# Optimization experiments

Measured on AMD Instinct MI355X. Metric: run time of the kernel, lower is better.

The kernel has to match this reference:

```python
import jax, jax.numpy as jnp
import numpy as np

B, Q, K, H = 4, 128, 1024, 256
QS, KS, DV = 256, 256, 256


def setup_inputs() -> dict:
    key = jax.random.key(0)
    k1, k2, k3, k4, k5, k6, k7 = jax.random.split(key, 7)
    return {
        "queries": jax.random.normal(k1, (B, Q, QS), dtype=jnp.float32),
        "keys": jax.random.normal(k2, (B, K, KS), dtype=jnp.float32),
        "values": jax.random.normal(k3, (B, K, DV), dtype=jnp.float32),
        "valid_lens": jax.random.randint(k4, (B,), 1, K, dtype=jnp.int64),
        "Wq": jax.random.normal(k5, (QS, H), dtype=jnp.float32) / np.sqrt(QS),
        "Wk": jax.random.normal(k6, (KS, H), dtype=jnp.float32) / np.sqrt(KS),
        "Wv": jax.random.normal(k7, (H,), dtype=jnp.float32) / np.sqrt(H),
    }


def reference(queries, keys, values, valid_lens, Wq, Wk, Wv):
    # Projections: [B,Q,H] and [B,K,H]
    q = jnp.einsum("bqe,eh->bqh", queries, Wq)
    k = jnp.einsum("bke,eh->bkh", keys, Wk)
    # Broadcast add + tanh: [B,Q,K,H] intermediate (the kernel-headroom op)
    feats = jnp.tanh(q[:, :, None, :] + k[:, None, :, :])
    # hidden -> 1 reduction: scores [B,Q,K]
    scores = jnp.einsum("bqkh,h->bqk", feats, Wv)
    # masked softmax: positions >= valid_len set to -1e6 (as in sequence_mask)
    mask = jnp.arange(scores.shape[-1])[None, None, :] < valid_lens[:, None, None]
    scores = jnp.where(mask, scores, jnp.float32(-1e6))
    attn = jax.nn.softmax(scores, axis=-1)
    # dropout is identity in eval mode
    return jnp.einsum("bqk,bkv->bqv", attn, values)
```

## Files before the change

### kernel.cpp

```cpp
#include <hip/hip_runtime.h>

#define NB 4
#define NQ 128
#define NK 1024
#define NH 256
#define NE 256
#define NV 256

#define TSCALE 2.8853900817779268f
#define LOG2E  1.4426950408889634f

static __device__ __forceinline__ float fexp2(float x){ return __builtin_amdgcn_exp2f(x); }
static __device__ __forceinline__ float frcp (float x){ return __builtin_amdgcn_rcpf(x); }
static __device__ __forceinline__ float tanh_of(float x){
    float e = fexp2(x * TSCALE);
    return fmaf(-2.0f, frcp(e + 1.0f), 1.0f);
}

__global__ __launch_bounds__(256) void proj_kernel(
    const float* __restrict__ qin, const float* __restrict__ kin,
    const float* __restrict__ Wq, const float* __restrict__ Wk,
    const float* __restrict__ Wv,
    float4* __restrict__ qdatA, float4* __restrict__ qdatB,
    float4* __restrict__ kT4) {
    const int tid = threadIdx.x;
    const int bi  = blockIdx.x;
    __shared__ float tr[NH][9];
    if (bi < NB * 32) {
        const int row0 = bi * 4;
        const float* r0 = qin + row0 * NE;
        float a0 = 0.f, a1 = 0.f, a2 = 0.f, a3 = 0.f;
#pragma unroll 2
        for (int e = 0; e < NE; e += 4) {
            float4 q0 = *(const float4*)(r0 + e);
            float4 q1 = *(const float4*)(r0 + NE + e);
            float4 q2 = *(const float4*)(r0 + 2 * NE + e);
            float4 q3 = *(const float4*)(r0 + 3 * NE + e);
#pragma unroll
            for (int j = 0; j < 4; ++j) {
                float w = Wq[(e + j) * NH + tid];
                a0 = fmaf(((const float*)&q0)[j], w, a0);
                a1 = fmaf(((const float*)&q1)[j], w, a1);
                a2 = fmaf(((const float*)&q2)[j], w, a2);
                a3 = fmaf(((const float*)&q3)[j], w, a3);
            }
        }
        float wv = Wv[tid];
        float t0 = tanh_of(a0), t1 = tanh_of(a1), t2 = tanh_of(a2), t3 = tanh_of(a3);
        qdatA[bi * NH + tid] = make_float4(t0, wv * t0, t1, wv * t1);
        qdatB[bi * NH + tid] = make_float4(t2, wv * t2, t3, wv * t3);
    } else {
        const int kb = bi - NB * 32;
        const int b  = kb >> 7;
        const int k0 = (kb & 127) * 8;
        const float* kr = kin + (b * NK + k0) * NE;
        float acc[8] = {0.f,0.f,0.f,0.f,0.f,0.f,0.f,0.f};
#pragma unroll 2
        for (int e = 0; e < NE; e += 4) {
            float4 kvv[8];
#pragma unroll
            for (int i = 0; i < 8; ++i) kvv[i] = *(const float4*)(kr + i * NE + e);
#pragma unroll
            for (int j = 0; j < 4; ++j) {
                float w = Wk[(e + j) * NH + tid];
#pragma unroll
                for (int i = 0; i < 8; ++i)
                    acc[i] = fmaf(((const float*)&kvv[i])[j], w, acc[i]);
            }
        }
#pragma unroll
        for (int i = 0; i < 8; ++i) tr[tid][i] = tanh_of(acc[i]);
        __syncthreads();
#pragma unroll
        for (int p = 0; p < 2; ++p) {
            int idx2 = p * 256 + tid;
            int hg = idx2 >> 3;
            int kk = idx2 & 7;
            float4 v = make_float4(tr[hg*4+0][kk], tr[hg*4+1][kk],
                                   tr[hg*4+2][kk], tr[hg*4+3][kk]);
            kT4[(b * 64 + hg) * NK + k0 + kk] = v;
        }
    }
}

__global__ __launch_bounds__(256) void attn_kernel(
    const float4* __restrict__ qdatA, const float4* __restrict__ qdatB,
    const float4* __restrict__ kT4, const float* __restrict__ V,
    const int* __restrict__ vlen, const float4* __restrict__ Wv4,
    float* __restrict__ part_m, float* __restrict__ part_s,
    float* __restrict__ part_pv) {
    const int tid = threadIdx.x, lane = tid & 63, wid = tid >> 6;
    const int bi = blockIdx.x;
    const int quarter = bi & 3;
    const int b  = (bi >> 2) & 3;
    const int qq = bi >> 4;
    const int vl = vlen[b];
    const int nch = (vl + 255) >> 8;
    const int pidx = (b * 32 + qq) * 4 + quarter;
    float* pm  = part_m + pidx * 4;
    float* ps  = part_s + pidx * 4;
    float* ppv = part_pv + pidx * (4 * NV);

    if (quarter >= nch) {
        if (tid < 4) { pm[tid] = -1e30f; ps[tid] = 0.0f; }
#pragma unroll
        for (int i = 0; i < 4; ++i) ppv[i * 256 + tid] = 0.0f;
        return;
    }

    __shared__ float  pw[4][NH];
    __shared__ float  pvred[4][64 * 17];
    __shared__ float  red[4][8];

    const float4* qA = qdatA + (b * 32 + qq) * NH;
    const float4* qB = qdatB + (b * 32 + qq) * NH;

    const int k = quarter * 256 + tid;
    const float4* kp = kT4 + (b * 64) * NK + k;
    float acc0 = 0.f, acc1 = 0.f, acc2 = 0.f, acc3 = 0.f;
#pragma unroll 4
    for (int h4 = 0; h4 < 64; ++h4) {
        float4 kv4 = kp[h4 * NK];
        float4 wv4 = Wv4[h4];
#pragma unroll
        for (int j = 0; j < 4; ++j) {
            float kv  = ((const float*)&kv4)[j];
            float wvb = ((const float*)&wv4)[j] * kv;
            float4 qa = qA[h4 * 4 + j];
            float4 qb = qB[h4 * 4 + j];
            acc0 = fmaf(qa.y + wvb, frcp(fmaf(qa.x, kv, 1.0f)), acc0);
            acc1 = fmaf(qa.w + wvb, frcp(fmaf(qa.z, kv, 1.0f)), acc1);
            acc2 = fmaf(qb.y + wvb, frcp(fmaf(qb.x, kv, 1.0f)), acc2);
            acc3 = fmaf(qb.w + wvb, frcp(fmaf(qb.z, kv, 1.0f)), acc3);
        }
    }
    const bool okk = k < vl;
    float s0 = okk ? acc0 : -1e30f;
    float s1 = okk ? acc1 : -1e30f;
    float s2 = okk ? acc2 : -1e30f;
    float s3 = okk ? acc3 : -1e30f;
    float m0 = s0, m1 = s1, m2 = s2, m3 = s3;
#pragma unroll
    for (int d = 32; d >= 1; d >>= 1) {
        m0 = fmaxf(m0, __shfl_xor(m0, d, 64));
        m1 = fmaxf(m1, __shfl_xor(m1, d, 64));
        m2 = fmaxf(m2, __shfl_xor(m2, d, 64));
        m3 = fmaxf(m3, __shfl_xor(m3, d, 64));
    }
    if (lane == 0) { red[wid][0]=m0; red[wid][1]=m1; red[wid][2]=m2; red[wid][3]=m3; }
    __syncthreads();
    m0 = fmaxf(fmaxf(red[0][0], red[1][0]), fmaxf(red[2][0], red[3][0]));
    m1 = fmaxf(fmaxf(red[0][1], red[1][1]), fmaxf(red[2][1], red[3][1]));
    m2 = fmaxf(fmaxf(red[0][2], red[1][2]), fmaxf(red[2][2], red[3][2]));
    m3 = fmaxf(fmaxf(red[0][3], red[1][3]), fmaxf(red[2][3], red[3][3]));
    float p0 = fexp2((s0 - m0) * LOG2E);
    float p1 = fexp2((s1 - m1) * LOG2E);
    float p2 = fexp2((s2 - m2) * LOG2E);
    float p3 = fexp2((s3 - m3) * LOG2E);
    pw[0][tid] = p0; pw[1][tid] = p1; pw[2][tid] = p2; pw[3][tid] = p3;
    float u0 = p0, u1 = p1, u2 = p2, u3 = p3;
#pragma unroll
    for (int d = 32; d >= 1; d >>= 1) {
        u0 += __shfl_xor(u0, d, 64); u1 += __shfl_xor(u1, d, 64);
        u2 += __shfl_xor(u2, d, 64); u3 += __shfl_xor(u3, d, 64);
    }
    if (lane == 0) { red[wid][4]=u0; red[wid][5]=u1; red[wid][6]=u2; red[wid][7]=u3; }
    __syncthreads();
    if (tid == 0) {
        pm[0] = m0; pm[1] = m1; pm[2] = m2; pm[3] = m3;
        ps[0] = red[0][4]+red[1][4]+red[2][4]+red[3][4];
        ps[1] = red[0][5]+red[1][5]+red[2][5]+red[3][5];
        ps[2] = red[0][6]+red[1][6]+red[2][6]+red[3][6];
        ps[3] = red[0][7]+red[1][7]+red[2][7]+red[3][7];
    }
    const float* Vb = V + (b * NK + quarter * 256) * NV;
    const int v4 = lane * 4;
    float4 o0 = {0,0,0,0}, o1 = {0,0,0,0}, o2 = {0,0,0,0}, o3 = {0,0,0,0};
    for (int kk0 = wid * 4; kk0 < 256; kk0 += 16) {
        float4 pr0 = *(const float4*)&pw[0][kk0];
        float4 pr1 = *(const float4*)&pw[1][kk0];
        float4 pr2 = *(const float4*)&pw[2][kk0];
        float4 pr3 = *(const float4*)&pw[3][kk0];
#pragma unroll
        for (int j = 0; j < 4; ++j) {
            float4 vv = *(const float4*)&Vb[(kk0 + j) * NV + v4];
            float w0 = ((const float*)&pr0)[j], w1 = ((const float*)&pr1)[j];
            float w2 = ((const float*)&pr2)[j], w3 = ((const float*)&pr3)[j];
            o0.x = fmaf(w0, vv.x, o0.x); o0.y = fmaf(w0, vv.y, o0.y);
            o0.z = fmaf(w0, vv.z, o0.z); o0.w = fmaf(w0, vv.w, o0.w);
            o1.x = fmaf(w1, vv.x, o1.x); o1.y = fmaf(w1, vv.y, o1.y);
            o1.z = fmaf(w1, vv.z, o1.z); o1.w = fmaf(w1, vv.w, o1.w);
            o2.x = fmaf(w2, vv.x, o2.x); o2.y = fmaf(w2, vv.y, o2.y);
            o2.z = fmaf(w2, vv.z, o2.z); o2.w = fmaf(w2, vv.w, o2.w);
            o3.x = fmaf(w3, vv.x, o3.x); o3.y = fmaf(w3, vv.y, o3.y);
            o3.z = fmaf(w3, vv.z, o3.z); o3.w = fmaf(w3, vv.w, o3.w);
        }
    }
    {
        float* pd = &pvred[wid][lane * 17];
        *(float4*)(pd + 0)  = o0;
        *(float4*)(pd + 4)  = o1;
        *(float4*)(pd + 8)  = o2;
        *(float4*)(pd + 12) = o3;
    }
    __syncthreads();
    {
        int row = tid >> 6, vg = tid & 63;
        float4 r = {0,0,0,0};
#pragma unroll
        for (int w = 0; w < 4; ++w) {
            float4 t = *(const float4*)&pvred[w][vg * 17 + row * 4];
            r.x += t.x; r.y += t.y; r.z += t.z; r.w += t.w;
        }
        *(float4*)&ppv[row * NV + vg * 4] = r;
    }
}

__global__ __launch_bounds__(256) void combine_kernel(
    const float* __restrict__ part_m, const float* __restrict__ part_s,
    const float* __restrict__ part_pv, float* __restrict__ out) {
    const int tid = threadIdx.x;
    const int bi  = blockIdx.x;
    const int base = bi * 4;
#pragma unroll
    for (int i = 0; i < 4; ++i) {
        float m[4], s[4];
#pragma unroll
        for (int q = 0; q < 4; ++q) {
            m[q] = part_m[(base + q) * 4 + i];
            s[q] = part_s[(base + q) * 4 + i];
        }
        float M = fmaxf(fmaxf(m[0], m[1]), fmaxf(m[2], m[3]));
        float w[4], S = 0.f;
#pragma unroll
        for (int q = 0; q < 4; ++q) {
            w[q] = fexp2((m[q] - M) * LOG2E);
            S = fmaf(s[q], w[q], S);
        }
        float o = 0.f;
#pragma unroll
        for (int q = 0; q < 4; ++q)
            o = fmaf(part_pv[((base + q) * 4 + i) * NV + tid], w[q], o);
        out[(base + i) * NV + tid] = o * frcp(S);
    }
}

extern "C" void kernel_launch(void* const* d_in, const int* in_sizes, int n_in,
                              void* d_out, int out_size, void* d_ws, size_t ws_size,
                              hipStream_t stream) {
    const float* queries = (const float*)d_in[0];
    const float* keys    = (const float*)d_in[1];
    const float* values  = (const float*)d_in[2];
    const int*   vlens   = (const int*)  d_in[3];
    const float* Wq      = (const float*)d_in[4];
    const float* Wk      = (const float*)d_in[5];
    const float* Wv      = (const float*)d_in[6];
    float* out = (float*)d_out;

    float4* qdatA  = (float4*)d_ws;
    float4* qdatB  = qdatA + NB * 32 * NH;
    float4* kT4    = qdatB + NB * 32 * NH;
    float*  part_m = (float*)(kT4 + NB * 64 * NK);
    float*  part_s = part_m + 2048;
    float*  part_pv = part_s + 2048;

    proj_kernel   <<<dim3(640), dim3(256), 0, stream>>>(queries, keys, Wq, Wk, Wv,
                                                        qdatA, qdatB, kT4);
    attn_kernel   <<<dim3(512), dim3(256), 0, stream>>>(qdatA, qdatB, kT4, values,
                                                        vlens, (const float4*)Wv,
                                                        part_m, part_s, part_pv);
    combine_kernel<<<dim3(128), dim3(256), 0, stream>>>(part_m, part_s, part_pv, out);
}
```

Measured before the change: 131.8 us.

## Compact attention grid to valid key chunks and batch four reciprocals into one

Blocks are now mapped in a packed order to only the (batch, query-group, key-chunk) tiles that fall inside each valid length. Inactive blocks exit at once and no longer write empty partials, so the combine kernel loops only over the valid chunk count. In the inner tanh-score loop, four reciprocals are replaced by one reciprocal of their product plus extra multiplies, cutting transcendental-unit pressure. The product of four denominators could overflow or underflow in float, which risks accuracy, and the combine loops are no longer unrolled.

```diff
diff --git a/kernel.cpp b/kernel.cpp
--- a/kernel.cpp
+++ b/kernel.cpp
@@ -90,23 +90,25 @@
     float* __restrict__ part_m, float* __restrict__ part_s,
     float* __restrict__ part_pv) {
     const int tid = threadIdx.x, lane = tid & 63, wid = tid >> 6;
-    const int bi = blockIdx.x;
-    const int quarter = bi & 3;
-    const int b  = (bi >> 2) & 3;
-    const int qq = bi >> 4;
-    const int vl = vlen[b];
-    const int nch = (vl + 255) >> 8;
+    const int n0 = (vlen[0] + 255) >> 8, n1 = (vlen[1] + 255) >> 8;
+    const int n2 = (vlen[2] + 255) >> 8, n3 = (vlen[3] + 255) >> 8;
+    const int c1 = 32 * n0, c2 = c1 + 32 * n1, c3 = c2 + 32 * n2;
+    const int W  = c3 + 32 * n3;
+    const int w  = blockIdx.x;
+    if (w >= W) return;
+    int b, base, nb;
+    if      (w >= c3) { b = 3; base = c3; nb = n3; }
+    else if (w >= c2) { b = 2; base = c2; nb = n2; }
+    else if (w >= c1) { b = 1; base = c1; nb = n1; }
+    else              { b = 0; base = 0;  nb = n0; }
+    const int rel     = w - base;
+    const int qq      = (unsigned)rel / (unsigned)nb;
+    const int quarter = rel - qq * nb;
+    const int vl      = vlen[b];
     const int pidx = (b * 32 + qq) * 4 + quarter;
     float* pm  = part_m + pidx * 4;
     float* ps  = part_s + pidx * 4;
     float* ppv = part_pv + pidx * (4 * NV);
-
-    if (quarter >= nch) {
-        if (tid < 4) { pm[tid] = -1e30f; ps[tid] = 0.0f; }
-#pragma unroll
-        for (int i = 0; i < 4; ++i) ppv[i * 256 + tid] = 0.0f;
-        return;
-    }
 
     __shared__ float  pw[4][NH];
     __shared__ float  pvred[4][64 * 17];
@@ -128,10 +130,18 @@
             float wvb = ((const float*)&wv4)[j] * kv;
             float4 qa = qA[h4 * 4 + j];
             float4 qb = qB[h4 * 4 + j];
-            acc0 = fmaf(qa.y + wvb, frcp(fmaf(qa.x, kv, 1.0f)), acc0);
-            acc1 = fmaf(qa.w + wvb, frcp(fmaf(qa.z, kv, 1.0f)), acc1);
-            acc2 = fmaf(qb.y + wvb, frcp(fmaf(qb.x, kv, 1.0f)), acc2);
-            acc3 = fmaf(qb.w + wvb, frcp(fmaf(qb.z, kv, 1.0f)), acc3);
+            float p0 = fmaf(qa.x, kv, 1.0f), nu0 = qa.y + wvb;
+            float p1 = fmaf(qa.z, kv, 1.0f), nu1 = qa.w + wvb;
+            float p2 = fmaf(qb.x, kv, 1.0f), nu2 = qb.y + wvb;
+            float p3 = fmaf(qb.z, kv, 1.0f), nu3 = qb.w + wvb;
+            float ab = p0 * p1, cd = p2 * p3;
+            float r  = frcp(ab * cd);
+            float rab = r * cd;
+            float rcd = r * ab;
+            acc0 = fmaf(nu0, rab * p1, acc0);
+            acc1 = fmaf(nu1, rab * p0, acc1);
+            acc2 = fmaf(nu2, rcd * p3, acc2);
+            acc3 = fmaf(nu3, rcd * p2, acc3);
         }
     }
     const bool okk = k < vl;
@@ -208,8 +218,8 @@
         int row = tid >> 6, vg = tid & 63;
         float4 r = {0,0,0,0};
 #pragma unroll
-        for (int w = 0; w < 4; ++w) {
-            float4 t = *(const float4*)&pvred[w][vg * 17 + row * 4];
+        for (int ww = 0; ww < 4; ++ww) {
+            float4 t = *(const float4*)&pvred[ww][vg * 17 + row * 4];
             r.x += t.x; r.y += t.y; r.z += t.z; r.w += t.w;
         }
         *(float4*)&ppv[row * NV + vg * 4] = r;
@@ -218,29 +228,30 @@
 
 __global__ __launch_bounds__(256) void combine_kernel(
     const float* __restrict__ part_m, const float* __restrict__ part_s,
-    const float* __restrict__ part_pv, float* __restrict__ out) {
+    const float* __restrict__ part_pv, const int* __restrict__ vlen,
+    float* __restrict__ out) {
     const int tid = threadIdx.x;
     const int bi  = blockIdx.x;
+    const int b   = bi >> 5;
+    const int nb  = (vlen[b] + 255) >> 8;
     const int base = bi * 4;
 #pragma unroll
     for (int i = 0; i < 4; ++i) {
         float m[4], s[4];
-#pragma unroll
-        for (int q = 0; q < 4; ++q) {
+        for (int q = 0; q < nb; ++q) {
             m[q] = part_m[(base + q) * 4 + i];
             s[q] = part_s[(base + q) * 4 + i];
         }
-        float M = fmaxf(fmaxf(m[0], m[1]), fmaxf(m[2], m[3]));
-        float w[4], S = 0.f;
-#pragma unroll
-        for (int q = 0; q < 4; ++q) {
-            w[q] = fexp2((m[q] - M) * LOG2E);
-            S = fmaf(s[q], w[q], S);
+        float M = m[0];
+        for (int q = 1; q < nb; ++q) M = fmaxf(M, m[q]);
+        float wq[4], S = 0.f;
+        for (int q = 0; q < nb; ++q) {
+            wq[q] = fexp2((m[q] - M) * LOG2E);
+            S = fmaf(s[q], wq[q], S);
         }
         float o = 0.f;
-#pragma unroll
-        for (int q = 0; q < 4; ++q)
-            o = fmaf(part_pv[((base + q) * 4 + i) * NV + tid], w[q], o);
+        for (int q = 0; q < nb; ++q)
+            o = fmaf(part_pv[((base + q) * 4 + i) * NV + tid], wq[q], o);
         out[(base + i) * NV + tid] = o * frcp(S);
     }
 }
@@ -269,5 +280,6 @@
     attn_kernel   <<<dim3(512), dim3(256), 0, stream>>>(qdatA, qdatB, kT4, values,
                                                         vlens, (const float4*)Wv,
                                                         part_m, part_s, part_pv);
-    combine_kernel<<<dim3(128), dim3(256), 0, stream>>>(part_m, part_s, part_pv, out);
-}
+    combine_kernel<<<dim3(128), dim3(256), 0, stream>>>(part_m, part_s, part_pv,
+                                                        vlens, out);
+}
```

Result: slower. 142.0 us (+7.7%).
